# Kernel optimization log

Hardware: AMD Instinct MI355X
Metric: run time of the kernel (lower is better)

The kernel has to match this reference:

```python
import jax, jax.numpy as jnp
import numpy as np
import math

FEAT_DIM, M, K = 512, 64, 256
D = FEAT_DIM // M  # 8
ALPHA = 1.0
B = 16384


def setup_inputs() -> dict:
    key = jax.random.key(0)
    kx, kc = jax.random.split(key)
    x = jax.random.normal(kx, (B, FEAT_DIM), dtype=jnp.float32)
    # Codebook: unit-norm codewords scaled by 1/sqrt(M), mimicking the
    # normalized-hypersphere init (orthogonal rotation / permutation do not
    # change the math, only the values).
    c = jax.random.normal(kc, (M, K, D), dtype=jnp.float32)
    c = c / jnp.linalg.norm(c, axis=-1, keepdims=True) / math.sqrt(M)
    return {"x": x, "C": c}


def reference(x, C):
    # x: (B, feat_dim) -> (B, M, D)
    x_ = x.reshape(x.shape[0], M, D)
    # per-subspace inner products with codewords: (B, M, K)
    ips = jnp.einsum('bmd,mkd->bmk', x_, C)
    # training-mode straight-through assignment
    soft = jax.nn.softmax(ips * (M / ALPHA), axis=-1)
    hard = jax.nn.one_hot(jnp.argmax(ips, axis=-1), K, dtype=ips.dtype)
    codes = jax.lax.stop_gradient(hard - soft) + soft
    # reconstruction: (B, M, D) -> (B, feat_dim)
    x_hat = jnp.einsum('mkd,bmk->bmd', C, codes).reshape(x.shape[0], -1)
    return x_hat, codes
```

## Files before the change

### kernel.cpp

```cpp
#include <hip/hip_runtime.h>
#include <math.h>


#define B_SZ   16384
#define FEAT   512
#define M_SZ   64
#define K_SZ   256
#define D_SZ   8

__global__ __launch_bounds__(256) void pq_argmax(
    const float* __restrict__ x,
    const float* __restrict__ C,
    unsigned char* __restrict__ bestk8)
{
#pragma clang fp contract(off)

    const int m     = blockIdx.x & (M_SZ - 1);
    const int chunk = blockIdx.x >> 6;
    const int t     = threadIdx.x;
    const int b     = (chunk << 8) | t;

    __shared__ float lC[K_SZ * D_SZ];
    {
        const float4* src = (const float4*)(C + (size_t)m * (K_SZ * D_SZ));
        float4* dst = (float4*)lC;
        dst[t]       = src[t];
        dst[t + 256] = src[t + 256];
    }
    __syncthreads();

    const float* xp = x + (size_t)b * FEAT + m * D_SZ;
    const float4 xa = *(const float4*)(xp);
    const float4 xb = *(const float4*)(xp + 4);

    float best  = -INFINITY;
    int   bestk = 0;

#pragma unroll 4
    for (int k = 0; k < K_SZ; ++k) {
        const float* cr = lC + k * D_SZ;
        float s0 = xa.x * cr[0];
        float s1 = xa.y * cr[1];
        float s2 = xa.z * cr[2];
        float s3 = xa.w * cr[3];
        float s4 = xb.x * cr[4];
        float s5 = xb.y * cr[5];
        float s6 = xb.z * cr[6];
        float s7 = xb.w * cr[7];
        float t0 = s0 + s4;
        float t1 = s1 + s5;
        float t2 = s2 + s6;
        float t3 = s3 + s7;
        float dot = (t0 + t1) + (t2 + t3);
        if (dot > best) { best = dot; bestk = k; }
    }

    bestk8[(size_t)b * M_SZ + m] = (unsigned char)bestk;
}

__global__ __launch_bounds__(256) void pq_write(
    const float* __restrict__ C,
    const unsigned char* __restrict__ bestk8,
    float* __restrict__ xhat,
    float* __restrict__ codes)
{
    const int tid  = blockIdx.x * blockDim.x + threadIdx.x;
    const int b    = tid >> 6;
    const int lane = threadIdx.x & 63;

    const int kb = (int)bestk8[(size_t)b * M_SZ + lane];

    {
        const float* cw = C + ((size_t)lane * K_SZ + kb) * D_SZ;
        const float4 h0 = *(const float4*)(cw);
        const float4 h1 = *(const float4*)(cw + 4);
        float* xh = xhat + (size_t)b * FEAT + lane * D_SZ;
        *(float4*)(xh)     = h0;
        *(float4*)(xh + 4) = h1;
    }

    const int lane4 = lane << 2;
    float* const base = codes + (size_t)b * (M_SZ * K_SZ) + lane4;
#pragma unroll 8
    for (int m = 0; m < M_SZ; ++m) {
        const int kj = __builtin_amdgcn_readlane(kb, m);
        float4 v;
        v.x = (kj == lane4 + 0) ? 1.0f : 0.0f;
        v.y = (kj == lane4 + 1) ? 1.0f : 0.0f;
        v.z = (kj == lane4 + 2) ? 1.0f : 0.0f;
        v.w = (kj == lane4 + 3) ? 1.0f : 0.0f;
        *(float4*)(base + (size_t)m * K_SZ) = v;
    }
}

extern "C" void kernel_launch(void* const* d_in, const int* in_sizes, int n_in,
                              void* d_out, int out_size, void* d_ws, size_t ws_size,
                              hipStream_t stream)
{
    const float* x = (const float*)d_in[0];
    const float* C = (const float*)d_in[1];
    float* xhat  = (float*)d_out;
    float* codes = (float*)d_out + (size_t)B_SZ * FEAT;
    unsigned char* bestk8 = (unsigned char*)d_ws;

    hipLaunchKernelGGL(pq_argmax, dim3(4096), dim3(256), 0, stream, x, C, bestk8);
    hipLaunchKernelGGL(pq_write,  dim3(4096), dim3(256), 0, stream, C, bestk8, xhat, codes);
}
```

Measured before the change: 1.212 ms.

## Read codebook from global, transpose code buffer, zero-fill codes then scatter ones

The argmax kernel drops the shared-memory codebook staging and its barrier, reading codewords straight from global memory through the cache, and the unroll factor rises from 4 to 8. The byte index buffer is transposed to m-major so each block's byte stores are contiguous. The write kernel now handles four rows per block: it zero-fills the whole codes slab with float4 stores, synchronises, then scatters a single 1.0 per (row, subspace). This removes the per-element compare work in the one-hot writes, but it adds a second, uncoalesced write after the zeros and replaces LDS reads with global loads in the inner loop.

```diff
diff --git a/kernel.cpp b/kernel.cpp
--- a/kernel.cpp
+++ b/kernel.cpp
@@ -17,28 +17,20 @@
 
     const int m     = blockIdx.x & (M_SZ - 1);
     const int chunk = blockIdx.x >> 6;
-    const int t     = threadIdx.x;
-    const int b     = (chunk << 8) | t;
-
-    __shared__ float lC[K_SZ * D_SZ];
-    {
-        const float4* src = (const float4*)(C + (size_t)m * (K_SZ * D_SZ));
-        float4* dst = (float4*)lC;
-        dst[t]       = src[t];
-        dst[t + 256] = src[t + 256];
-    }
-    __syncthreads();
+    const int b     = (chunk << 8) | threadIdx.x;
 
     const float* xp = x + (size_t)b * FEAT + m * D_SZ;
     const float4 xa = *(const float4*)(xp);
     const float4 xb = *(const float4*)(xp + 4);
 
+    const float* __restrict__ Cm = C + (size_t)m * (K_SZ * D_SZ);
+
     float best  = -INFINITY;
     int   bestk = 0;
 
-#pragma unroll 4
+#pragma unroll 8
     for (int k = 0; k < K_SZ; ++k) {
-        const float* cr = lC + k * D_SZ;
+        const float* cr = Cm + k * D_SZ;
         float s0 = xa.x * cr[0];
         float s1 = xa.y * cr[1];
         float s2 = xa.z * cr[2];
@@ -55,7 +47,7 @@
         if (dot > best) { best = dot; bestk = k; }
     }
 
-    bestk8[(size_t)b * M_SZ + m] = (unsigned char)bestk;
+    bestk8[(size_t)m * B_SZ + b] = (unsigned char)bestk;
 }
 
 __global__ __launch_bounds__(256) void pq_write(
@@ -64,33 +56,33 @@
     float* __restrict__ xhat,
     float* __restrict__ codes)
 {
-    const int tid  = blockIdx.x * blockDim.x + threadIdx.x;
-    const int b    = tid >> 6;
-    const int lane = threadIdx.x & 63;
+    const int t    = threadIdx.x;
+    const int b0   = blockIdx.x << 2;
+    const int r    = t >> 6;
+    const int lane = t & 63;
+    const int b    = b0 + r;
 
-    const int kb = (int)bestk8[(size_t)b * M_SZ + lane];
+    const int kb = (int)bestk8[(size_t)lane * B_SZ + b];
 
     {
         const float* cw = C + ((size_t)lane * K_SZ + kb) * D_SZ;
-        const float4 h0 = *(const float4*)(cw);
-        const float4 h1 = *(const float4*)(cw + 4);
+        const float4 h0 = ((const float4*)cw)[0];
+        const float4 h1 = ((const float4*)cw)[1];
         float* xh = xhat + (size_t)b * FEAT + lane * D_SZ;
-        *(float4*)(xh)     = h0;
-        *(float4*)(xh + 4) = h1;
+        ((float4*)xh)[0] = h0;
+        ((float4*)xh)[1] = h1;
     }
 
-    const int lane4 = lane << 2;
-    float* const base = codes + (size_t)b * (M_SZ * K_SZ) + lane4;
+    {
+        const float4 z = {0.f, 0.f, 0.f, 0.f};
+        float4* slab = (float4*)(codes + (size_t)b0 * (M_SZ * K_SZ));
 #pragma unroll 8
-    for (int m = 0; m < M_SZ; ++m) {
-        const int kj = __builtin_amdgcn_readlane(kb, m);
-        float4 v;
-        v.x = (kj == lane4 + 0) ? 1.0f : 0.0f;
-        v.y = (kj == lane4 + 1) ? 1.0f : 0.0f;
-        v.z = (kj == lane4 + 2) ? 1.0f : 0.0f;
-        v.w = (kj == lane4 + 3) ? 1.0f : 0.0f;
-        *(float4*)(base + (size_t)m * K_SZ) = v;
+        for (int i = t; i < 16384; i += 256) slab[i] = z;
     }
+
+    __syncthreads();
+
+    codes[((size_t)b * M_SZ + lane) * K_SZ + kb] = 1.0f;
 }
 
 extern "C" void kernel_launch(void* const* d_in, const int* in_sizes, int n_in,
```

Result: slower. 1.256 ms (+3.6%).
